# Kernel optimization log

Measured on AMD Instinct MI355X. Metric: run time of the kernel, lower is better.

The kernel has to match this reference:

```python
import jax, jax.numpy as jnp
import numpy as np
from jax import lax

LBDA = 0.5   # soft-min temperature from OTAM_cum_dist_v2 default
EPS = 0.01   # cos_sim epsilon


def otam_cum_dist(dists, lbda=LBDA):
    """Soft-DTW-style OTAM DP. dists: [nq, ns, L, S] -> [nq, ns].
    Faithful to OTAM_cum_dist_v2: pad last dim by (1,1) with zeros, then run the
    row-wise recurrence. Soft-min computed via stable logsumexp (same math as
    -lbda*log(sum exp(-x/lbda)))."""
    nq, ns, L, S = dists.shape
    d = jnp.pad(dists, ((0, 0), (0, 0), (0, 0), (1, 1)))  # [nq, ns, L, W], W=S+2
    W = S + 2
    # Row 0: cum[0, m] = cum[0, m-1] + d[0, m], cum[0, 0] = 0
    row0 = jnp.concatenate(
        [jnp.zeros((nq, ns, 1), d.dtype), jnp.cumsum(d[:, :, 0, 1:], axis=-1)], axis=-1)
    if L == 1:
        return row0[..., -1]

    m_idx = jnp.arange(1, W)
    include_up = (m_idx == 1) | (m_idx == W - 1)  # only first/last cols use cum[l-1, m]
    INF = jnp.asarray(jnp.inf, d.dtype)

    def row_step(prev_row, d_row):
        # prev_row, d_row: [nq, ns, W]
        xs = (
            jnp.moveaxis(d_row[:, :, 1:], -1, 0),        # d[l, m],       [W-1, nq, ns]
            jnp.moveaxis(prev_row[:, :, :-1], -1, 0),    # cum[l-1, m-1]
            jnp.moveaxis(prev_row[:, :, 1:], -1, 0),     # cum[l-1, m]
            include_up,
        )

        def col_step(cur_left, x):
            d_m, p_diag, p_up, inc = x
            up = jnp.where(inc, p_up, INF)               # masked term -> exp(-inf)=0
            terms = jnp.stack([p_diag, cur_left, up])    # [3, nq, ns]
            new = d_m - lbda * jax.nn.logsumexp(-terms / lbda, axis=0)
            return new, new

        _, cols = lax.scan(col_step, jnp.zeros((nq, ns), d.dtype), xs)
        row = jnp.concatenate(
            [jnp.zeros((nq, ns, 1), d.dtype), jnp.moveaxis(cols, 0, -1)], axis=-1)
        return row, None

    d_rows = jnp.moveaxis(d[:, :, 1:, :], 2, 0)          # [L-1, nq, ns, W]
    final_row, _ = lax.scan(row_step, row0, d_rows)
    return final_row[..., -1]


def reference(support_features, query_features):
    """OTAM meta-logits (cum_dist_g = -otam_distance) of DSN_TEMPORAL.
    support_features: [n_classes, L, D] class prototypes; query_features: [nq, L, D]."""
    nq, Lq, D = query_features.shape
    ns, Ls, _ = support_features.shape
    q = query_features.reshape(nq * Lq, D)
    s = support_features.reshape(ns * Ls, D)
    # cos_sim with epsilon in denominator (faithful to cos_sim())
    num = q @ s.T
    den = (jnp.linalg.norm(q, axis=-1)[:, None]
           * jnp.linalg.norm(s, axis=-1)[None, :] + EPS)
    frame_dists = 1.0 - num / den                         # [nq*L, ns*S]
    dists = frame_dists.reshape(nq, Lq, ns, Ls).transpose(0, 2, 1, 3)  # [nq, ns, L, S]
    cum = otam_cum_dist(dists) + otam_cum_dist(dists.transpose(0, 1, 3, 2))
    return -cum                                           # meta_logits [nq, ns]


def setup_inputs() -> dict:
    key = jax.random.key(0)
    k1, k2 = jax.random.split(key)
    return {
        "support_features": jax.random.normal(k1, (64, 8, 576), dtype=jnp.float32),
        "query_features": jax.random.normal(k2, (2048, 8, 576), dtype=jnp.float32),
    }
```

## Files before the change

kernel.cpp:

```cpp
#include <hip/hip_runtime.h>

#define D_K 576
#define LBDA_INV 2.0f
#define HALF_LBDA 0.5f
#define EPS 0.01f
#define LDA 40
#define DSTRIDE 136

typedef __attribute__((ext_vector_type(8))) short short8;
typedef __attribute__((ext_vector_type(4))) short short4v;
typedef __attribute__((ext_vector_type(4))) float f32x4;

__device__ inline short f2bf(float f) {
    unsigned u = __float_as_uint(f);
    u += 0x7FFF + ((u >> 16) & 1);
    return (short)(u >> 16);
}
__device__ inline float bf2f(unsigned short s) {
    return __uint_as_float(((unsigned)s) << 16);
}

__global__ __launch_bounds__(256) void norms_kernel(
        const float* __restrict__ sup, const float* __restrict__ qry,
        float* __restrict__ qn, float* __restrict__ sn) {
    int t = threadIdx.x;
    int row = blockIdx.x * 4 + (t >> 6);
    int lane = t & 63;
    const float* base = (row < 16384) ? (qry + (size_t)row * D_K)
                                      : (sup + (size_t)(row - 16384) * D_K);
    float s = 0.f;
#pragma unroll
    for (int i = 0; i < 9; ++i) {
        float v = base[lane + i * 64];
        s += v * v;
    }
#pragma unroll
    for (int off = 32; off > 0; off >>= 1)
        s += __shfl_down(s, off);
    if (lane == 0) {
        float r = sqrtf(s);
        if (row < 16384) qn[row] = r;
        else sn[row - 16384] = r;
    }
}

__device__ inline float softmin3(float a, float b, float c) {
    float mn = fminf(a, fminf(b, c));
    float s = __expf(-LBDA_INV * (a - mn)) + __expf(-LBDA_INV * (b - mn)) +
              __expf(-LBDA_INV * (c - mn));
    return mn - HALF_LBDA * __logf(s);
}
__device__ inline float softmin2(float a, float b) {
    float mn = fminf(a, b);
    float s = __expf(-LBDA_INV * (a - mn)) + __expf(-LBDA_INV * (b - mn));
    return mn - HALF_LBDA * __logf(s);
}

template <int RS, int CS>
__device__ float otam_dp(const float* d) {
    float prev[10], cur[10];
    prev[0] = 0.f;
#pragma unroll
    for (int m = 1; m <= 8; ++m) prev[m] = prev[m - 1] + d[0 * RS + (m - 1) * CS];
    prev[9] = prev[8];
#pragma unroll
    for (int l = 1; l < 8; ++l) {
        cur[0] = 0.f;
        cur[1] = d[l * RS + 0 * CS] + softmin3(prev[0], 0.f, prev[1]);
#pragma unroll
        for (int m = 2; m <= 8; ++m)
            cur[m] = d[l * RS + (m - 1) * CS] + softmin2(prev[m - 1], cur[m - 1]);
        cur[9] = softmin3(prev[8], cur[8], prev[9]);
#pragma unroll
        for (int m = 0; m < 10; ++m) prev[m] = cur[m];
    }
    return prev[9];
}

__global__ __launch_bounds__(256, 2) void fused_kernel(
        const float* __restrict__ sup, const float* __restrict__ qry,
        const float* __restrict__ qn, const float* __restrict__ sn,
        float* __restrict__ out) {
    __shared__ short As[128 * LDA];
    __shared__ short Bs[128 * LDA];
    __shared__ unsigned short Ds[128 * DSTRIDE];

    const int t = threadIdx.x;
    const int sblk = blockIdx.x;
    const int qblk = blockIdx.y;

    const float* Ag = qry + (size_t)qblk * 128 * D_K;
    const float* Bg = sup + (size_t)sblk * 128 * D_K;

    const int lane = t & 63;
    const int wave = t >> 6;
    const int wm = wave >> 1, wn = wave & 1;
    const int col16 = lane & 15, quad = lane >> 4;

    f32x4 acc[4][4];
#pragma unroll
    for (int i = 0; i < 4; ++i)
#pragma unroll
        for (int j = 0; j < 4; ++j) acc[i][j] = (f32x4){0.f, 0.f, 0.f, 0.f};

    for (int k0 = 0; k0 < D_K; k0 += 32) {
        __syncthreads();
#pragma unroll
        for (int i = 0; i < 4; ++i) {
            int idx = t + i * 256;
            int r = idx >> 3, c = idx & 7;
            const float4 va = *(const float4*)(Ag + (size_t)r * D_K + k0 + c * 4);
            short4v sa = {f2bf(va.x), f2bf(va.y), f2bf(va.z), f2bf(va.w)};
            *(short4v*)(&As[r * LDA + c * 4]) = sa;
            const float4 vb = *(const float4*)(Bg + (size_t)r * D_K + k0 + c * 4);
            short4v sb = {f2bf(vb.x), f2bf(vb.y), f2bf(vb.z), f2bf(vb.w)};
            *(short4v*)(&Bs[r * LDA + c * 4]) = sb;
        }
        __syncthreads();

        short8 af[4], bf[4];
#pragma unroll
        for (int mt = 0; mt < 4; ++mt)
            af[mt] = *(const short8*)(&As[(wm * 64 + mt * 16 + col16) * LDA + quad * 8]);
#pragma unroll
        for (int nt = 0; nt < 4; ++nt)
            bf[nt] = *(const short8*)(&Bs[(wn * 64 + nt * 16 + col16) * LDA + quad * 8]);
#pragma unroll
        for (int mt = 0; mt < 4; ++mt)
#pragma unroll
            for (int nt = 0; nt < 4; ++nt)
                acc[mt][nt] = __builtin_amdgcn_mfma_f32_16x16x32_bf16(
                    af[mt], bf[nt], acc[mt][nt], 0, 0, 0);
    }

#pragma unroll
    for (int mt = 0; mt < 4; ++mt) {
#pragma unroll
        for (int reg = 0; reg < 4; ++reg) {
            int m = wm * 64 + mt * 16 + quad * 4 + reg;
            float qv = qn[qblk * 128 + m];
#pragma unroll
            for (int nt = 0; nt < 4; ++nt) {
                int n = wn * 64 + nt * 16 + col16;
                float sv = sn[sblk * 128 + n];
                float dist = 1.f - acc[mt][nt][reg] / (qv * sv + EPS);
                Ds[m * DSTRIDE + n] = (unsigned short)f2bf(dist);
            }
        }
    }
    __syncthreads();

    const int ql = t >> 4, sl = t & 15;
    float d[64];
#pragma unroll
    for (int l = 0; l < 8; ++l) {
        short8 rowv = *(const short8*)(&Ds[(ql * 8 + l) * DSTRIDE + sl * 8]);
#pragma unroll
        for (int j = 0; j < 8; ++j) d[l * 8 + j] = bf2f((unsigned short)rowv[j]);
    }
    float r1 = otam_dp<8, 1>(d);
    float r2 = otam_dp<1, 8>(d);
    int qg = qblk * 16 + ql, sg = sblk * 16 + sl;
    out[qg * 64 + sg] = -(r1 + r2);
}

extern "C" void kernel_launch(void* const* d_in, const int* in_sizes, int n_in,
                              void* d_out, int out_size, void* d_ws, size_t ws_size,
                              hipStream_t stream) {
    const float* sup = (const float*)d_in[0];
    const float* qry = (const float*)d_in[1];
    float* out = (float*)d_out;
    float* qn = (float*)d_ws;
    float* sn = qn + 16384;

    norms_kernel<<<dim3((16384 + 512) / 4), dim3(256), 0, stream>>>(sup, qry, qn, sn);
    fused_kernel<<<dim3(4, 128), dim3(256), 0, stream>>>(sup, qry, qn, sn, out);
}
```

Before: 116.8 us.

## Pre-convert inputs to bf16 and stream GEMM tiles via global_load_lds

The prep kernel now computes the norms and also writes bf16 copies of the query and support features to workspace. The fused kernel then loads those bf16 tiles straight into LDS with global_load_lds, using a k-chunk-major layout, instead of converting fp32 to bf16 per tile inside the GEMM loop. It also remaps the 1D grid so query blocks are grouped per XCD for L2 locality. The cost is an extra bf16 write and read pass through memory, and the new LDS layout may bring bank conflicts on the fragment reads.

After: 117.4 us. No clear change (+0.5%).

```diff
diff --git a/kernel.cpp b/kernel.cpp
--- a/kernel.cpp
+++ b/kernel.cpp
@@ -4,8 +4,10 @@
 #define LBDA_INV 2.0f
 #define HALF_LBDA 0.5f
 #define EPS 0.01f
-#define LDA 40
 #define DSTRIDE 136
+
+#define NQROW 16384
+#define NSROW 512
 
 typedef __attribute__((ext_vector_type(8))) short short8;
 typedef __attribute__((ext_vector_type(4))) short short4v;
@@ -20,27 +22,39 @@
     return __uint_as_float(((unsigned)s) << 16);
 }
 
-__global__ __launch_bounds__(256) void norms_kernel(
+__device__ inline void load_lds16(const void* g, void* l) {
+    __builtin_amdgcn_global_load_lds(
+        (const __attribute__((address_space(1))) unsigned int*)g,
+        (__attribute__((address_space(3))) unsigned int*)l,
+        16, 0, 0);
+}
+
+__global__ __launch_bounds__(256) void prep_kernel(
         const float* __restrict__ sup, const float* __restrict__ qry,
+        unsigned short* __restrict__ qb, unsigned short* __restrict__ sb,
         float* __restrict__ qn, float* __restrict__ sn) {
     int t = threadIdx.x;
     int row = blockIdx.x * 4 + (t >> 6);
     int lane = t & 63;
-    const float* base = (row < 16384) ? (qry + (size_t)row * D_K)
-                                      : (sup + (size_t)(row - 16384) * D_K);
+    bool isq = row < NQROW;
+    const float* base = isq ? (qry + (size_t)row * D_K)
+                            : (sup + (size_t)(row - NQROW) * D_K);
+    unsigned short* dst = isq ? (qb + (size_t)row * D_K)
+                              : (sb + (size_t)(row - NQROW) * D_K);
     float s = 0.f;
-#pragma unroll
-    for (int i = 0; i < 9; ++i) {
-        float v = base[lane + i * 64];
-        s += v * v;
+    for (int c = lane; c < 144; c += 64) {
+        float4 v = *(const float4*)(base + c * 4);
+        s += v.x * v.x + v.y * v.y + v.z * v.z + v.w * v.w;
+        short4v o = {f2bf(v.x), f2bf(v.y), f2bf(v.z), f2bf(v.w)};
+        *(short4v*)(dst + c * 4) = o;
     }
 #pragma unroll
     for (int off = 32; off > 0; off >>= 1)
         s += __shfl_down(s, off);
     if (lane == 0) {
         float r = sqrtf(s);
-        if (row < 16384) qn[row] = r;
-        else sn[row - 16384] = r;
+        if (isq) qn[row] = r;
+        else sn[row - NQROW] = r;
     }
 }
 
@@ -78,19 +92,21 @@
 }
 
 __global__ __launch_bounds__(256, 2) void fused_kernel(
-        const float* __restrict__ sup, const float* __restrict__ qry,
+        const unsigned short* __restrict__ qb, const unsigned short* __restrict__ sb,
         const float* __restrict__ qn, const float* __restrict__ sn,
         float* __restrict__ out) {
-    __shared__ short As[128 * LDA];
-    __shared__ short Bs[128 * LDA];
+    __shared__ unsigned short As[512 * 8];
+    __shared__ unsigned short Bs[512 * 8];
     __shared__ unsigned short Ds[128 * DSTRIDE];
 
     const int t = threadIdx.x;
-    const int sblk = blockIdx.x;
-    const int qblk = blockIdx.y;
+    const int b = blockIdx.x;
+    const int xcd = b & 7, s = b >> 3;
+    const int sblk = s >> 4;
+    const int qblk = xcd * 16 + (s & 15);
 
-    const float* Ag = qry + (size_t)qblk * 128 * D_K;
-    const float* Bg = sup + (size_t)sblk * 128 * D_K;
+    const unsigned short* Ag = qb + (size_t)qblk * 128 * D_K;
+    const unsigned short* Bg = sb + (size_t)sblk * 128 * D_K;
 
     const int lane = t & 63;
     const int wave = t >> 6;
@@ -104,33 +120,33 @@
         for (int j = 0; j < 4; ++j) acc[i][j] = (f32x4){0.f, 0.f, 0.f, 0.f};
 
     for (int k0 = 0; k0 < D_K; k0 += 32) {
-        __syncthreads();
 #pragma unroll
-        for (int i = 0; i < 4; ++i) {
-            int idx = t + i * 256;
-            int r = idx >> 3, c = idx & 7;
-            const float4 va = *(const float4*)(Ag + (size_t)r * D_K + k0 + c * 4);
-            short4v sa = {f2bf(va.x), f2bf(va.y), f2bf(va.z), f2bf(va.w)};
-            *(short4v*)(&As[r * LDA + c * 4]) = sa;
-            const float4 vb = *(const float4*)(Bg + (size_t)r * D_K + k0 + c * 4);
-            short4v sb = {f2bf(vb.x), f2bf(vb.y), f2bf(vb.z), f2bf(vb.w)};
-            *(short4v*)(&Bs[r * LDA + c * 4]) = sb;
+        for (int i = 0; i < 2; ++i) {
+            int p = wave * 64 + i * 256 + lane;
+            int r = p & 127, c = p >> 7;
+            load_lds16(Ag + (size_t)r * D_K + k0 + c * 8, &As[(wave * 64 + i * 256) * 8]);
+            load_lds16(Bg + (size_t)r * D_K + k0 + c * 8, &Bs[(wave * 64 + i * 256) * 8]);
         }
         __syncthreads();
 
         short8 af[4], bf[4];
 #pragma unroll
-        for (int mt = 0; mt < 4; ++mt)
-            af[mt] = *(const short8*)(&As[(wm * 64 + mt * 16 + col16) * LDA + quad * 8]);
+        for (int mt = 0; mt < 4; ++mt) {
+            int row = wm * 64 + mt * 16 + col16;
+            af[mt] = *(const short8*)(&As[(quad * 128 + row) * 8]);
+        }
 #pragma unroll
-        for (int nt = 0; nt < 4; ++nt)
-            bf[nt] = *(const short8*)(&Bs[(wn * 64 + nt * 16 + col16) * LDA + quad * 8]);
+        for (int nt = 0; nt < 4; ++nt) {
+            int row = wn * 64 + nt * 16 + col16;
+            bf[nt] = *(const short8*)(&Bs[(quad * 128 + row) * 8]);
+        }
 #pragma unroll
         for (int mt = 0; mt < 4; ++mt)
 #pragma unroll
             for (int nt = 0; nt < 4; ++nt)
                 acc[mt][nt] = __builtin_amdgcn_mfma_f32_16x16x32_bf16(
                     af[mt], bf[nt], acc[mt][nt], 0, 0, 0);
+        __syncthreads();
     }
 
 #pragma unroll
@@ -170,9 +186,13 @@
     const float* sup = (const float*)d_in[0];
     const float* qry = (const float*)d_in[1];
     float* out = (float*)d_out;
-    float* qn = (float*)d_ws;
-    float* sn = qn + 16384;
 
-    norms_kernel<<<dim3((16384 + 512) / 4), dim3(256), 0, stream>>>(sup, qry, qn, sn);
-    fused_kernel<<<dim3(4, 128), dim3(256), 0, stream>>>(sup, qry, qn, sn, out);
+    unsigned short* qb = (unsigned short*)d_ws;
+    unsigned short* sb = qb + (size_t)NQROW * D_K;
+    float* qn = (float*)(sb + (size_t)NSROW * D_K);
+    float* sn = qn + NQROW;
+
+    prep_kernel<<<dim3((NQROW + NSROW) / 4), dim3(256), 0, stream>>>(
+        sup, qry, qb, sb, qn, sn);
+    fused_kernel<<<dim3(512), dim3(256), 0, stream>>>(qb, sb, qn, sn, out);
 }
```

## Pre-convert inputs to MFMA-friendly bf16 slabs and load fragments directly from global

Applied to the files above, without the earlier changes.

A prep kernel now converts query and support features to bf16 once, stores them in a slab layout matching the MFMA fragment access pattern, and writes partial sums of squares per slab. The fused kernel then reads fragments straight from global memory, so the LDS staging and per-iteration barriers are gone, and it finishes the norms locally. It also remaps block indices so query tiles group by XCD for better L2 reuse. The cost is writing and re-reading an extra bf16 workspace, and the GEMM operands now come from global memory or cache instead of LDS.

Result: faster. 110.7 us (-5.2%).

```diff
diff --git a/kernel.cpp b/kernel.cpp
--- a/kernel.cpp
+++ b/kernel.cpp
@@ -1,11 +1,19 @@
 #include <hip/hip_runtime.h>
 
 #define D_K 576
+#define NSLAB 18
 #define LBDA_INV 2.0f
 #define HALF_LBDA 0.5f
 #define EPS 0.01f
-#define LDA 40
 #define DSTRIDE 136
+
+#define NQROW 16384
+#define NSROW 512
+#define NQT 128
+#define NST 4
+#define NT 132
+#define TILE_ELEMS (128 * D_K)
+#define SLAB_ELEMS (128 * 32)
 
 typedef __attribute__((ext_vector_type(8))) short short8;
 typedef __attribute__((ext_vector_type(4))) short short4v;
@@ -20,28 +28,36 @@
     return __uint_as_float(((unsigned)s) << 16);
 }
 
-__global__ __launch_bounds__(256) void norms_kernel(
+__global__ __launch_bounds__(256) void prep_kernel(
         const float* __restrict__ sup, const float* __restrict__ qry,
-        float* __restrict__ qn, float* __restrict__ sn) {
-    int t = threadIdx.x;
-    int row = blockIdx.x * 4 + (t >> 6);
-    int lane = t & 63;
-    const float* base = (row < 16384) ? (qry + (size_t)row * D_K)
-                                      : (sup + (size_t)(row - 16384) * D_K);
-    float s = 0.f;
-#pragma unroll
-    for (int i = 0; i < 9; ++i) {
-        float v = base[lane + i * 64];
-        s += v * v;
-    }
-#pragma unroll
-    for (int off = 32; off > 0; off >>= 1)
-        s += __shfl_down(s, off);
-    if (lane == 0) {
-        float r = sqrtf(s);
-        if (row < 16384) qn[row] = r;
-        else sn[row - 16384] = r;
-    }
+        unsigned short* __restrict__ tb, float* __restrict__ psum) {
+    __shared__ unsigned short Ls[SLAB_ELEMS];
+    const int t = threadIdx.x;
+    const int slab = blockIdx.x;
+    const int tile = blockIdx.y;
+    const bool isq = tile < NQT;
+    const float* src = (isq ? qry + (size_t)tile * 128 * D_K
+                            : sup + (size_t)(tile - NQT) * 128 * D_K) + slab * 32;
+    float* ps = psum + ((size_t)tile * NSLAB + slab) * 128;
+
+#pragma unroll
+    for (int i = 0; i < 4; ++i) {
+        int idx = i * 256 + t;
+        int r = idx >> 3, c = idx & 7;
+        float4 v = *(const float4*)(src + (size_t)r * D_K + c * 4);
+        float ss = v.x * v.x + v.y * v.y + v.z * v.z + v.w * v.w;
+        ss += __shfl_down(ss, 4);
+        ss += __shfl_down(ss, 2);
+        ss += __shfl_down(ss, 1);
+        if ((t & 7) == 0) ps[r] = ss;
+        int c_in = c >> 1, half = c & 1;
+        short4v o = {f2bf(v.x), f2bf(v.y), f2bf(v.z), f2bf(v.w)};
+        *(short4v*)(&Ls[(c_in * 128 + r) * 8 + half * 4]) = o;
+    }
+    __syncthreads();
+    unsigned short* dst = tb + (size_t)tile * TILE_ELEMS + (size_t)slab * SLAB_ELEMS;
+    *(short8*)(dst + t * 16) = *(const short8*)(&Ls[t * 16]);
+    *(short8*)(dst + t * 16 + 8) = *(const short8*)(&Ls[t * 16 + 8]);
 }
 
 __device__ inline float softmin3(float a, float b, float c) {
@@ -78,19 +94,36 @@
 }
 
 __global__ __launch_bounds__(256, 2) void fused_kernel(
-        const float* __restrict__ sup, const float* __restrict__ qry,
-        const float* __restrict__ qn, const float* __restrict__ sn,
+        const unsigned short* __restrict__ tb, const float* __restrict__ psum,
         float* __restrict__ out) {
-    __shared__ short As[128 * LDA];
-    __shared__ short Bs[128 * LDA];
     __shared__ unsigned short Ds[128 * DSTRIDE];
+    __shared__ float qn_l[128], sn_l[128];
 
     const int t = threadIdx.x;
-    const int sblk = blockIdx.x;
-    const int qblk = blockIdx.y;
-
-    const float* Ag = qry + (size_t)qblk * 128 * D_K;
-    const float* Bg = sup + (size_t)sblk * 128 * D_K;
+    const int b = blockIdx.x;
+    const int xcd = b & 7, s2 = b >> 3;
+    const int sblk = s2 >> 4;
+    const int qblk = xcd * 16 + (s2 & 15);
+
+    {
+        const float* pq = psum + (size_t)qblk * NSLAB * 128;
+        const float* ps = psum + (size_t)(NQT + sblk) * NSLAB * 128;
+        if (t < 128) {
+            float a = 0.f;
+#pragma unroll
+            for (int sl = 0; sl < NSLAB; ++sl) a += pq[sl * 128 + t];
+            qn_l[t] = sqrtf(a);
+        } else {
+            int r = t - 128;
+            float a = 0.f;
+#pragma unroll
+            for (int sl = 0; sl < NSLAB; ++sl) a += ps[sl * 128 + r];
+            sn_l[r] = sqrtf(a);
+        }
+    }
+
+    const unsigned short* At = tb + (size_t)qblk * TILE_ELEMS;
+    const unsigned short* Bt = tb + (size_t)(NQT + sblk) * TILE_ELEMS;
 
     const int lane = t & 63;
     const int wave = t >> 6;
@@ -103,28 +136,23 @@
 #pragma unroll
         for (int j = 0; j < 4; ++j) acc[i][j] = (f32x4){0.f, 0.f, 0.f, 0.f};
 
-    for (int k0 = 0; k0 < D_K; k0 += 32) {
-        __syncthreads();
-#pragma unroll
-        for (int i = 0; i < 4; ++i) {
-            int idx = t + i * 256;
-            int r = idx >> 3, c = idx & 7;
-            const float4 va = *(const float4*)(Ag + (size_t)r * D_K + k0 + c * 4);
-            short4v sa = {f2bf(va.x), f2bf(va.y), f2bf(va.z), f2bf(va.w)};
-            *(short4v*)(&As[r * LDA + c * 4]) = sa;
-            const float4 vb = *(const float4*)(Bg + (size_t)r * D_K + k0 + c * 4);
-            short4v sb = {f2bf(vb.x), f2bf(vb.y), f2bf(vb.z), f2bf(vb.w)};
-            *(short4v*)(&Bs[r * LDA + c * 4]) = sb;
-        }
-        __syncthreads();
-
+    int aoff[4], boff[4];
+#pragma unroll
+    for (int mt = 0; mt < 4; ++mt)
+        aoff[mt] = (quad * 128 + wm * 64 + mt * 16 + col16) * 8;
+#pragma unroll
+    for (int nt = 0; nt < 4; ++nt)
+        boff[nt] = (quad * 128 + wn * 64 + nt * 16 + col16) * 8;
+
+#pragma unroll 3
+    for (int sl = 0; sl < NSLAB; ++sl) {
+        const unsigned short* Asl = At + sl * SLAB_ELEMS;
+        const unsigned short* Bsl = Bt + sl * SLAB_ELEMS;
         short8 af[4], bf[4];
 #pragma unroll
-        for (int mt = 0; mt < 4; ++mt)
-            af[mt] = *(const short8*)(&As[(wm * 64 + mt * 16 + col16) * LDA + quad * 8]);
-#pragma unroll
-        for (int nt = 0; nt < 4; ++nt)
-            bf[nt] = *(const short8*)(&Bs[(wn * 64 + nt * 16 + col16) * LDA + quad * 8]);
+        for (int mt = 0; mt < 4; ++mt) af[mt] = *(const short8*)(Asl + aoff[mt]);
+#pragma unroll
+        for (int nt = 0; nt < 4; ++nt) bf[nt] = *(const short8*)(Bsl + boff[nt]);
 #pragma unroll
         for (int mt = 0; mt < 4; ++mt)
 #pragma unroll
@@ -132,17 +160,18 @@
                 acc[mt][nt] = __builtin_amdgcn_mfma_f32_16x16x32_bf16(
                     af[mt], bf[nt], acc[mt][nt], 0, 0, 0);
     }
+    __syncthreads();
 
 #pragma unroll
     for (int mt = 0; mt < 4; ++mt) {
 #pragma unroll
         for (int reg = 0; reg < 4; ++reg) {
             int m = wm * 64 + mt * 16 + quad * 4 + reg;
-            float qv = qn[qblk * 128 + m];
+            float qv = qn_l[m];
 #pragma unroll
             for (int nt = 0; nt < 4; ++nt) {
                 int n = wn * 64 + nt * 16 + col16;
-                float sv = sn[sblk * 128 + n];
+                float sv = sn_l[n];
                 float dist = 1.f - acc[mt][nt][reg] / (qv * sv + EPS);
                 Ds[m * DSTRIDE + n] = (unsigned short)f2bf(dist);
             }
@@ -170,9 +199,10 @@
     const float* sup = (const float*)d_in[0];
     const float* qry = (const float*)d_in[1];
     float* out = (float*)d_out;
-    float* qn = (float*)d_ws;
-    float* sn = qn + 16384;
-
-    norms_kernel<<<dim3((16384 + 512) / 4), dim3(256), 0, stream>>>(sup, qry, qn, sn);
-    fused_kernel<<<dim3(4, 128), dim3(256), 0, stream>>>(sup, qry, qn, sn, out);
-}
+
+    unsigned short* tb = (unsigned short*)d_ws;
+    float* psum = (float*)(tb + (size_t)NT * TILE_ELEMS);
+
+    prep_kernel<<<dim3(NSLAB, NT), dim3(256), 0, stream>>>(sup, qry, tb, psum);
+    fused_kernel<<<dim3(512), dim3(256), 0, stream>>>(tb, psum, out);
+}
```

## Fuse norm computation into GEMM tile loads and remap blocks per XCD

Applied to the files above, without the earlier changes.

Removes the separate norms kernel and computes squared row norms from the fp32 values already loaded for the bf16 GEMM tiles, reducing them with shuffles into shared memory. It also changes the LDS layout to a k-chunk-major XOR-swizzled arrangement, aliases the distance buffer onto the A/B tile buffers to cut LDS use, and uses packed bf16 conversion intrinsics. Block indices are remapped so that the query blocks sharing an XCD are grouped together, aiming for better L2 reuse. The cost is an extra barrier per k-slab and some extra FMA work in the load path.

Measured after the change: 126.1 us. 1.08x slower.

```diff
diff --git a/kernel.cpp b/kernel.cpp
--- a/kernel.cpp
+++ b/kernel.cpp
@@ -1,47 +1,22 @@
 #include <hip/hip_runtime.h>
+#include <hip/hip_bf16.h>
 
 #define D_K 576
+#define NSLAB 18
 #define LBDA_INV 2.0f
 #define HALF_LBDA 0.5f
 #define EPS 0.01f
-#define LDA 40
 #define DSTRIDE 136
 
 typedef __attribute__((ext_vector_type(8))) short short8;
-typedef __attribute__((ext_vector_type(4))) short short4v;
 typedef __attribute__((ext_vector_type(4))) float f32x4;
 
-__device__ inline short f2bf(float f) {
-    unsigned u = __float_as_uint(f);
-    u += 0x7FFF + ((u >> 16) & 1);
-    return (short)(u >> 16);
-}
 __device__ inline float bf2f(unsigned short s) {
     return __uint_as_float(((unsigned)s) << 16);
 }
-
-__global__ __launch_bounds__(256) void norms_kernel(
-        const float* __restrict__ sup, const float* __restrict__ qry,
-        float* __restrict__ qn, float* __restrict__ sn) {
-    int t = threadIdx.x;
-    int row = blockIdx.x * 4 + (t >> 6);
-    int lane = t & 63;
-    const float* base = (row < 16384) ? (qry + (size_t)row * D_K)
-                                      : (sup + (size_t)(row - 16384) * D_K);
-    float s = 0.f;
-#pragma unroll
-    for (int i = 0; i < 9; ++i) {
-        float v = base[lane + i * 64];
-        s += v * v;
-    }
-#pragma unroll
-    for (int off = 32; off > 0; off >>= 1)
-        s += __shfl_down(s, off);
-    if (lane == 0) {
-        float r = sqrtf(s);
-        if (row < 16384) qn[row] = r;
-        else sn[row - 16384] = r;
-    }
+__device__ inline unsigned pack_bf16(float x, float y) {
+    __hip_bfloat162 h = __float22bfloat162_rn(float2{x, y});
+    return *reinterpret_cast<unsigned*>(&h);
 }
 
 __device__ inline float softmin3(float a, float b, float c) {
@@ -79,15 +54,18 @@
 
 __global__ __launch_bounds__(256, 2) void fused_kernel(
         const float* __restrict__ sup, const float* __restrict__ qry,
-        const float* __restrict__ qn, const float* __restrict__ sn,
         float* __restrict__ out) {
-    __shared__ short As[128 * LDA];
-    __shared__ short Bs[128 * LDA];
-    __shared__ unsigned short Ds[128 * DSTRIDE];
+    __shared__ unsigned short smem[128 * DSTRIDE];
+    __shared__ float qn_l[128], sn_l[128];
+    unsigned short* As = smem;
+    unsigned short* Bs = smem + 4096;
+    unsigned short* Ds = smem;
 
     const int t = threadIdx.x;
-    const int sblk = blockIdx.x;
-    const int qblk = blockIdx.y;
+    const int b = blockIdx.x;
+    const int xcd = b & 7, s2 = b >> 3;
+    const int sblk = s2 >> 4;
+    const int qblk = xcd * 16 + (s2 & 15);
 
     const float* Ag = qry + (size_t)qblk * 128 * D_K;
     const float* Bg = sup + (size_t)sblk * 128 * D_K;
@@ -103,48 +81,93 @@
 #pragma unroll
         for (int j = 0; j < 4; ++j) acc[i][j] = (f32x4){0.f, 0.f, 0.f, 0.f};
 
-    for (int k0 = 0; k0 < D_K; k0 += 32) {
-        __syncthreads();
+    const int srow = t >> 3, scol = t & 7;
+    const int c_in = scol >> 1, half = scol & 1;
+    const int swz = c_in << 1;
+    float sq_a[4] = {0.f, 0.f, 0.f, 0.f}, sq_b[4] = {0.f, 0.f, 0.f, 0.f};
+
+    int aoff[4], boff[4];
+#pragma unroll
+    for (int mt = 0; mt < 4; ++mt) {
+        int m = wm * 64 + mt * 16 + col16;
+        aoff[mt] = (quad * 128 + (m ^ (quad << 1))) * 8;
+    }
+#pragma unroll
+    for (int nt = 0; nt < 4; ++nt) {
+        int n = wn * 64 + nt * 16 + col16;
+        boff[nt] = (quad * 128 + (n ^ (quad << 1))) * 8;
+    }
+
+    for (int j = 0; j < NSLAB; ++j) {
+        const int kbase = j * 32 + scol * 4;
+        float4 va[4], vb[4];
 #pragma unroll
         for (int i = 0; i < 4; ++i) {
-            int idx = t + i * 256;
-            int r = idx >> 3, c = idx & 7;
-            const float4 va = *(const float4*)(Ag + (size_t)r * D_K + k0 + c * 4);
-            short4v sa = {f2bf(va.x), f2bf(va.y), f2bf(va.z), f2bf(va.w)};
-            *(short4v*)(&As[r * LDA + c * 4]) = sa;
-            const float4 vb = *(const float4*)(Bg + (size_t)r * D_K + k0 + c * 4);
-            short4v sb = {f2bf(vb.x), f2bf(vb.y), f2bf(vb.z), f2bf(vb.w)};
-            *(short4v*)(&Bs[r * LDA + c * 4]) = sb;
+            int r = i * 32 + srow;
+            va[i] = *(const float4*)(Ag + (size_t)r * D_K + kbase);
+            vb[i] = *(const float4*)(Bg + (size_t)r * D_K + kbase);
+        }
+#pragma unroll
+        for (int i = 0; i < 4; ++i) {
+            int r = i * 32 + srow;
+            int off = (c_in * 128 + (r ^ swz)) * 8 + half * 4;
+            sq_a[i] += va[i].x * va[i].x + va[i].y * va[i].y +
+                       va[i].z * va[i].z + va[i].w * va[i].w;
+            sq_b[i] += vb[i].x * vb[i].x + vb[i].y * vb[i].y +
+                       vb[i].z * vb[i].z + vb[i].w * vb[i].w;
+            *(uint2*)(As + off) = uint2{pack_bf16(va[i].x, va[i].y),
+                                        pack_bf16(va[i].z, va[i].w)};
+            *(uint2*)(Bs + off) = uint2{pack_bf16(vb[i].x, vb[i].y),
+                                        pack_bf16(vb[i].z, vb[i].w)};
         }
         __syncthreads();
 
         short8 af[4], bf[4];
 #pragma unroll
-        for (int mt = 0; mt < 4; ++mt)
-            af[mt] = *(const short8*)(&As[(wm * 64 + mt * 16 + col16) * LDA + quad * 8]);
+        for (int mt = 0; mt < 4; ++mt) af[mt] = *(const short8*)(As + aoff[mt]);
 #pragma unroll
-        for (int nt = 0; nt < 4; ++nt)
-            bf[nt] = *(const short8*)(&Bs[(wn * 64 + nt * 16 + col16) * LDA + quad * 8]);
+        for (int nt = 0; nt < 4; ++nt) bf[nt] = *(const short8*)(Bs + boff[nt]);
 #pragma unroll
         for (int mt = 0; mt < 4; ++mt)
 #pragma unroll
             for (int nt = 0; nt < 4; ++nt)
                 acc[mt][nt] = __builtin_amdgcn_mfma_f32_16x16x32_bf16(
                     af[mt], bf[nt], acc[mt][nt], 0, 0, 0);
+        __syncthreads();
     }
+
+#pragma unroll
+    for (int i = 0; i < 4; ++i) {
+        sq_a[i] += __shfl_down(sq_a[i], 4);
+        sq_a[i] += __shfl_down(sq_a[i], 2);
+        sq_a[i] += __shfl_down(sq_a[i], 1);
+        sq_b[i] += __shfl_down(sq_b[i], 4);
+        sq_b[i] += __shfl_down(sq_b[i], 2);
+        sq_b[i] += __shfl_down(sq_b[i], 1);
+    }
+    if ((t & 7) == 0) {
+        int r = t >> 3;
+#pragma unroll
+        for (int i = 0; i < 4; ++i) {
+            qn_l[i * 32 + r] = sqrtf(sq_a[i]);
+            sn_l[i * 32 + r] = sqrtf(sq_b[i]);
+        }
+    }
+    __syncthreads();
 
 #pragma unroll
     for (int mt = 0; mt < 4; ++mt) {
 #pragma unroll
         for (int reg = 0; reg < 4; ++reg) {
             int m = wm * 64 + mt * 16 + quad * 4 + reg;
-            float qv = qn[qblk * 128 + m];
+            float qv = qn_l[m];
 #pragma unroll
             for (int nt = 0; nt < 4; ++nt) {
                 int n = wn * 64 + nt * 16 + col16;
-                float sv = sn[sblk * 128 + n];
+                float sv = sn_l[n];
                 float dist = 1.f - acc[mt][nt][reg] / (qv * sv + EPS);
-                Ds[m * DSTRIDE + n] = (unsigned short)f2bf(dist);
+                unsigned p = pack_bf16(dist, 0.f);
+                Ds[m * DSTRIDE + n] = (unsigned short)(p & 0xFFFF);
             }
         }
     }
@@ -156,7 +179,7 @@
     for (int l = 0; l < 8; ++l) {
         short8 rowv = *(const short8*)(&Ds[(ql * 8 + l) * DSTRIDE + sl * 8]);
 #pragma unroll
-        for (int j = 0; j < 8; ++j) d[l * 8 + j] = bf2f((unsigned short)rowv[j]);
+        for (int jj = 0; jj < 8; ++jj) d[l * 8 + jj] = bf2f((unsigned short)rowv[jj]);
     }
     float r1 = otam_dp<8, 1>(d);
     float r2 = otam_dp<1, 8>(d);
@@ -170,9 +193,5 @@
     const float* sup = (const float*)d_in[0];
     const float* qry = (const float*)d_in[1];
     float* out = (float*)d_out;
-    float* qn = (float*)d_ws;
-    float* sn = qn + 16384;
-
-    norms_kernel<<<dim3((16384 + 512) / 4), dim3(256), 0, stream>>>(sup, qry, qn, sn);
-    fused_kernel<<<dim3(4, 128), dim3(256), 0, stream>>>(sup, qry, qn, sn, out);
+    fused_kernel<<<dim3(512), dim3(256), 0, stream>>>(sup, qry, out);
 }
```
